# Optimization experiments

Hardware: AMD Instinct MI355X
Metric: run time of the kernel (lower is better)

Reference implementation:

```python
import jax, jax.numpy as jnp
import numpy as np

B = 4096; CPG = 2; NPC = 25              # graphs, components/graph, nodes/component
N = B * CPG * NPC; C = B * CPG; E = 409600
IN_CH = 128; HID = 256; L = 3; S = 64; M = 8; NCLS = 2
BN_EPS = 1e-5

def _leaky(x):
    return jax.nn.leaky_relu(x, 0.01)

def _gin_conv(x, src, dst, wa, ba, wb, bb):
    # GINConv with eps=0: mlp(x + sum_{j in N(i)} x_j); messages flow src->dst
    agg = jnp.zeros_like(x).at[dst].add(x[src])
    h = x + agg
    return jax.nn.relu(h @ wa + ba) @ wb + bb

def setup_inputs():
    key = jax.random.key(0)
    ks = jax.random.split(key, 12)
    rn = lambda k, shp: jax.random.normal(k, shp, jnp.float32) * 0.05
    return {
        "x": jax.random.normal(ks[0], (N, IN_CH), jnp.float32),
        "w0a": rn(ks[1], (IN_CH, HID)), "b0a": jnp.zeros((HID,), jnp.float32),
        "w0b": rn(ks[2], (HID, HID)), "b0b": jnp.zeros((HID,), jnp.float32),
        "wra": rn(ks[3], (L - 1, HID, HID)), "bra": jnp.zeros((L - 1, HID), jnp.float32),
        "wrb": rn(ks[4], (L - 1, HID, HID)), "brb": jnp.zeros((L - 1, HID), jnp.float32),
        "Wc": jax.random.uniform(ks[5], (HID, S * M), jnp.float32, -1.0, 1.0),
        "fc1_w": rn(ks[6], (S, 32)), "fc1_b": jnp.zeros((32,), jnp.float32),
        "bn_g": jnp.ones((32,), jnp.float32), "bn_b": jnp.zeros((32,), jnp.float32),
        "fc2_w": rn(ks[7], (32, NCLS)), "fc2_b": jnp.zeros((NCLS,), jnp.float32),
        "edge_index": jax.random.randint(ks[8], (2, E), 0, N, jnp.int32),
        "node2comp": (jnp.arange(N, dtype=jnp.int32) // NPC),
        "comp2graph": (jnp.arange(C, dtype=jnp.int32) // CPG),
        "comp_pos": (jnp.arange(C, dtype=jnp.int32) % CPG),
        "n_graphs": B,
        "max_comps": CPG,
    }

def reference(x, w0a, b0a, w0b, b0b, wra, bra, wrb, brb, Wc, fc1_w, fc1_b, bn_g, bn_b, fc2_w, fc2_b, edge_index, node2comp, comp2graph, comp_pos, n_graphs, max_comps):
    src, dst = edge_index[0], edge_index[1]
    # --- GIN backbone (num_layers convs, ReLU between layers) ---
    h = _gin_conv(x, src, dst, w0a, b0a, w0b, b0b)
    for i in range(wra.shape[0]):
        h = jax.nn.relu(h)
        h = _gin_conv(h, src, dst, wra[i], bra[i], wrb[i], brb[i])
    # --- per-connected-component mean pooling ---
    n_comp = comp2graph.shape[0]
    comp_sum = jax.ops.segment_sum(h, node2comp, num_segments=n_comp)           # [C, d]
    comp_size = jax.ops.segment_sum(jnp.ones((h.shape[0],), h.dtype), node2comp, num_segments=n_comp)
    # torch.mean over the zero-padded cardinality dim divides by the per-graph MAX component size
    graph_maxc = jax.ops.segment_max(comp_size, comp2graph, num_segments=n_graphs)
    comp_mean = comp_sum / graph_maxc[comp2graph][:, None]
    # --- pad components into [B, max_comps, d] ---
    X = jnp.zeros((n_graphs, max_comps, h.shape[1]), h.dtype).at[comp2graph, comp_pos].set(comp_mean)
    # --- set-rep classifier ---
    t = _leaky(jnp.einsum('bcd,dk->bck', X, Wc))                                # [B, maxC, S*M]
    s = fc1_w.shape[0]; m = Wc.shape[1] // s
    t = t.reshape(t.shape[0], t.shape[1], m, s)                                 # view(B, maxC, n_elements, n_hidden_sets)
    t = jnp.max(t, axis=2)
    t = jnp.sum(t, axis=1)                                                      # [B, S]
    t = t @ fc1_w + fc1_b
    mu = jnp.mean(t, axis=0); var = jnp.var(t, axis=0)                          # BN, batch stats (track_running_stats=False)
    t = (t - mu) / jnp.sqrt(var + BN_EPS) * bn_g + bn_b
    t = _leaky(t)
    out = t @ fc2_w + fc2_b
    return jax.nn.log_softmax(out, axis=1)
```

## Files before the change

### kernel.cpp

```cpp
#include <hip/hip_runtime.h>
#include <hip/hip_fp16.h>
#include <math.h>

typedef unsigned short u16;
typedef float f32x4 __attribute__((ext_vector_type(4)));
typedef __bf16 bf16x8 __attribute__((ext_vector_type(8)));

__device__ __forceinline__ float b2f(u16 u) {
    union { unsigned int i; float f; } v; v.i = ((unsigned int)u) << 16; return v.f;
}
__device__ __forceinline__ u16 f2b(float f) {
    union { float f; unsigned int i; } v; v.f = f;
    unsigned int lsb = (v.i >> 16) & 1u;
    return (u16)((v.i + 0x7fffu + lsb) >> 16);
}
__device__ __forceinline__ unsigned int cvtpk(float lo, float hi) {
    unsigned int r;
    asm("v_cvt_pk_bf16_f32 %0, %1, %2" : "=v"(r) : "v"(lo), "v"(hi));
    return r;
}

__global__ __launch_bounds__(256)
void k_scan1(const int* __restrict__ cnt, int* __restrict__ rowptr,
             int* __restrict__ bsum, int N)
{
    __shared__ int s[256];
    int t = threadIdx.x, i = blockIdx.x * 256 + t;
    int v = (i < N) ? cnt[i] : 0;
    s[t] = v;
    __syncthreads();
#pragma unroll
    for (int off = 1; off < 256; off <<= 1) {
        int add = (t >= off) ? s[t - off] : 0;
        __syncthreads();
        s[t] += add;
        __syncthreads();
    }
    if (i < N) rowptr[i] = s[t] - v;
    if (t == 255) bsum[blockIdx.x] = s[255];
}

__global__ __launch_bounds__(256)
void k_scan2(const int* __restrict__ bsum, int* __restrict__ bscan, int nb)
{
    __shared__ int s[256];
    int t = threadIdx.x;
    int g[4], e[4];
    int base = t * 4;
#pragma unroll
    for (int j = 0; j < 4; ++j) g[j] = (base + j < nb) ? bsum[base + j] : 0;
    e[0] = 0; e[1] = g[0]; e[2] = g[0] + g[1]; e[3] = g[0] + g[1] + g[2];
    int tsum = e[3] + g[3];
    s[t] = tsum;
    __syncthreads();
#pragma unroll
    for (int off = 1; off < 256; off <<= 1) {
        int add = (t >= off) ? s[t - off] : 0;
        __syncthreads();
        s[t] += add;
        __syncthreads();
    }
    int texcl = s[t] - tsum;
#pragma unroll
    for (int j = 0; j < 4; ++j)
        if (base + j < nb) bscan[base + j] = texcl + e[j];
}

__global__ __launch_bounds__(256)
void k_scan3(int* __restrict__ rowptr, const int* __restrict__ bscan,
             int* __restrict__ cursor, int N)
{
    int i = blockIdx.x * 256 + threadIdx.x;
    if (i >= N) return;
    int r = rowptr[i] + bscan[i >> 8];
    rowptr[i] = r;
    cursor[i] = r;
}

__global__ __launch_bounds__(256)
void k_fill(const int* __restrict__ src, const int* __restrict__ dst,
            int* __restrict__ cursor, int* __restrict__ col, int E)
{
    int e = blockIdx.x * 256 + threadIdx.x;
    if (e >= E) return;
    int pos = atomicAdd(&cursor[dst[e]], 1);
    col[pos] = src[e];
}

__global__ __launch_bounds__(256)
void k_setup(const float* __restrict__ w0a, const float* __restrict__ w0b,
             const float* __restrict__ wra, const float* __restrict__ wrb,
             const float* __restrict__ Wc,  u16* __restrict__ wt,
             const int* __restrict__ dst, int* __restrict__ cnt, int E)
{
    int t = blockIdx.x * 256 + threadIdx.x;
    if (t < E) atomicAdd(&cnt[dst[t]], 1);

    const float* in; u16* out; int K, N, l;
    if      (t < 32768)  { in = w0a;          out = wt;          K = 128; N = 256; l = t; }
    else if (t < 98304)  { in = w0b;          out = wt + 65536;  K = 256; N = 256; l = t - 32768; }
    else if (t < 163840) { in = wra;          out = wt + 131072; K = 256; N = 256; l = t - 98304; }
    else if (t < 229376) { in = wra + 65536;  out = wt + 196608; K = 256; N = 256; l = t - 163840; }
    else if (t < 294912) { in = wrb;          out = wt + 262144; K = 256; N = 256; l = t - 229376; }
    else if (t < 360448) { in = wrb + 65536;  out = wt + 327680; K = 256; N = 256; l = t - 294912; }
    else if (t < 491520) { in = Wc;           out = wt + 393216; K = 256; N = 512; l = t - 360448; }
    else return;
    out[l] = f2b(in[(l % K) * N + l / K]);
}

#define CCAP 512

template<int K, bool RELU, bool F32SRC>
__global__ __launch_bounds__(512, 6)
void k_gin(const void* __restrict__ hsrc,
           const int* __restrict__ cnt, const int* __restrict__ rowptr,
           const int* __restrict__ col,
           const u16* __restrict__ WaT, const float* __restrict__ ba,
           const u16* __restrict__ WbT, const float* __restrict__ bb,
           u16* __restrict__ Hout, int Ntot, int Etot)
{
    __shared__ u16 AH[64 * 256];
    __shared__ int colLDS[CCAP];

    const int tid = threadIdx.x, lane = tid & 63, wave = tid >> 6;
    const int bm0 = blockIdx.x * 64;
    const int lc = lane & 15, lr = (lane >> 4) * 4;
    const int cw0 = wave * 32;
    const int l15 = lane & 15, lq = lane >> 4;

    const int rp0 = rowptr[bm0];
    const int rpE = (bm0 + 64 < Ntot) ? rowptr[bm0 + 64] : Etot;
    const int total = rpE - rp0;
    for (int i = tid; i < total && i < CCAP; i += 512) colLDS[i] = col[rp0 + i];

    bf16x8 bpre0 = *(const bf16x8*)(WaT + (size_t)(cw0 + l15) * K + lq * 8);
    bf16x8 bpre1 = *(const bf16x8*)(WaT + (size_t)(cw0 + 16 + l15) * K + lq * 8);
    __syncthreads();

    {
        constexpr int NSEG = K / 8;
        const int gr = tid >> 3, gseg = tid & 7;
        const int node = bm0 + gr;
        const int nn = cnt[node], rp = rowptr[node];
        const int jbase = rp - rp0;
        const int nIt = nn + 1;

        float acc[NSEG];
#pragma unroll
        for (int i = 0; i < NSEG; ++i) acc[i] = 0.f;

        if (F32SRC) {
            const float4* bp = (const float4*)hsrc;
            const int stride = K / 4, off = gseg * (NSEG / 4);
            const float4* p = bp + (size_t)node * stride + off;
            float4 a0 = p[0], a1 = p[1];
            for (int t = 0; t < nIt; ++t) {
                float4 b0 = p[2], b1 = p[3];
                int tn = (t + 1 < nIt) ? t + 1 : t;
                int jl = jbase + tn - 1;
                int idxN = (tn == 0) ? node : ((jl < CCAP) ? colLDS[jl] : col[rp + tn - 1]);
                const float4* q = bp + (size_t)idxN * stride + off;
                float4 n0 = q[0], n1 = q[1];
                if (RELU) {
                    acc[0] += fmaxf(a0.x,0.f); acc[1] += fmaxf(a0.y,0.f); acc[2] += fmaxf(a0.z,0.f); acc[3] += fmaxf(a0.w,0.f);
                    acc[4] += fmaxf(a1.x,0.f); acc[5] += fmaxf(a1.y,0.f); acc[6] += fmaxf(a1.z,0.f); acc[7] += fmaxf(a1.w,0.f);
                    acc[8] += fmaxf(b0.x,0.f); acc[9] += fmaxf(b0.y,0.f); acc[10]+= fmaxf(b0.z,0.f); acc[11]+= fmaxf(b0.w,0.f);
                    acc[12]+= fmaxf(b1.x,0.f); acc[13]+= fmaxf(b1.y,0.f); acc[14]+= fmaxf(b1.z,0.f); acc[15]+= fmaxf(b1.w,0.f);
                } else {
                    acc[0] += a0.x; acc[1] += a0.y; acc[2] += a0.z; acc[3] += a0.w;
                    acc[4] += a1.x; acc[5] += a1.y; acc[6] += a1.z; acc[7] += a1.w;
                    acc[8] += b0.x; acc[9] += b0.y; acc[10]+= b0.z; acc[11]+= b0.w;
                    acc[12]+= b1.x; acc[13]+= b1.y; acc[14]+= b1.z; acc[15]+= b1.w;
                }
                a0 = n0; a1 = n1; p = q;
            }
        } else {
            const uint4* bp = (const uint4*)hsrc;
            const int stride = K / 8, off = gseg * (NSEG / 8);
            const uint4* p = bp + (size_t)node * stride + off;
            uint4 a0 = p[0], a1 = p[1];
            for (int t = 0; t < nIt; ++t) {
                uint4 b0 = p[2], b1 = p[3];
                int tn = (t + 1 < nIt) ? t + 1 : t;
                int jl = jbase + tn - 1;
                int idxN = (tn == 0) ? node : ((jl < CCAP) ? colLDS[jl] : col[rp + tn - 1]);
                const uint4* q = bp + (size_t)idxN * stride + off;
                uint4 n0 = q[0], n1 = q[1];
                u16 vs[32] __attribute__((aligned(16)));
                *(uint4*)(vs + 0)  = a0; *(uint4*)(vs + 8)  = a1;
                *(uint4*)(vs + 16) = b0; *(uint4*)(vs + 24) = b1;
#pragma unroll
                for (int i2 = 0; i2 < 32; ++i2) {
                    float x = b2f(vs[i2]);
                    acc[i2] += RELU ? fmaxf(x, 0.f) : x;
                }
                a0 = n0; a1 = n1; p = q;
            }
        }

        const int k0 = gseg * NSEG;
        constexpr int NKC = NSEG / 8;
#pragma unroll
        for (int cc = 0; cc < NKC; ++cc) {
            const int k = k0 + cc * 8;
            const int s  = (k >> 5) * 256 + (gr >> 4) * 64 + ((k >> 3) & 3) * 16 + (gr & 15);
            const int sp = s ^ ((k >> 5) & 7);
            uint4 pk;
            pk.x = cvtpk(acc[cc * 8 + 0], acc[cc * 8 + 1]);
            pk.y = cvtpk(acc[cc * 8 + 2], acc[cc * 8 + 3]);
            pk.z = cvtpk(acc[cc * 8 + 4], acc[cc * 8 + 5]);
            pk.w = cvtpk(acc[cc * 8 + 6], acc[cc * 8 + 7]);
            *(uint4*)(AH + sp * 8) = pk;
        }
    }
    __syncthreads();

    constexpr int NK1 = K / 32;
    f32x4 acc1[4][2];
#pragma unroll
    for (int r = 0; r < 4; ++r)
#pragma unroll
        for (int c = 0; c < 2; ++c) acc1[r][c] = (f32x4){0.f, 0.f, 0.f, 0.f};

#pragma unroll
    for (int kb = 0; kb < NK1; ++kb) {
        bf16x8 a[4], b[2];
        if (kb == 0) { b[0] = bpre0; b[1] = bpre1; }
        else {
#pragma unroll
            for (int c = 0; c < 2; ++c)
                b[c] = *(const bf16x8*)(WaT + (size_t)(cw0 + c * 16 + l15) * K + kb * 32 + lq * 8);
        }
#pragma unroll
        for (int r = 0; r < 4; ++r)
            a[r] = *(const bf16x8*)&AH[(kb * 256 + r * 64 + (lane ^ (kb & 7))) * 8];
        __builtin_amdgcn_s_setprio(1);
#pragma unroll
        for (int r = 0; r < 4; ++r)
#pragma unroll
            for (int c = 0; c < 2; ++c)
                acc1[r][c] = __builtin_amdgcn_mfma_f32_16x16x32_bf16(a[r], b[c], acc1[r][c], 0, 0, 0);
        __builtin_amdgcn_s_setprio(0);
    }
    __syncthreads();

#pragma unroll
    for (int c = 0; c < 2; ++c) {
        const int n = cw0 + c * 16 + lc;
        const float bv = ba[n];
        const int nb = (n >> 5) * 256 + ((n >> 3) & 3) * 16;
        const int sx = (n >> 5) & 7;
#pragma unroll
        for (int r = 0; r < 4; ++r)
#pragma unroll
            for (int i = 0; i < 4; ++i) {
                const int sp = (nb + r * 64 + lr + i) ^ sx;
                AH[sp * 8 + (n & 7)] = f2b(fmaxf(acc1[r][c][i] + bv, 0.f));
            }
    }
    __syncthreads();

    f32x4 acc2[4][2];
#pragma unroll
    for (int r = 0; r < 4; ++r)
#pragma unroll
        for (int c = 0; c < 2; ++c) acc2[r][c] = (f32x4){0.f, 0.f, 0.f, 0.f};

#pragma unroll
    for (int kb = 0; kb < 8; ++kb) {
        bf16x8 a[4], b[2];
#pragma unroll
        for (int c = 0; c < 2; ++c)
            b[c] = *(const bf16x8*)(WbT + (size_t)(cw0 + c * 16 + l15) * 256 + kb * 32 + lq * 8);
#pragma unroll
        for (int r = 0; r < 4; ++r)
            a[r] = *(const bf16x8*)&AH[(kb * 256 + r * 64 + (lane ^ (kb & 7))) * 8];
        __builtin_amdgcn_s_setprio(1);
#pragma unroll
        for (int r = 0; r < 4; ++r)
#pragma unroll
            for (int c = 0; c < 2; ++c)
                acc2[r][c] = __builtin_amdgcn_mfma_f32_16x16x32_bf16(a[r], b[c], acc2[r][c], 0, 0, 0);
        __builtin_amdgcn_s_setprio(0);
    }
#pragma unroll
    for (int c = 0; c < 2; ++c) {
        const int n = cw0 + c * 16 + lc;
        const float bv = bb[n];
#pragma unroll
        for (int r = 0; r < 4; ++r)
#pragma unroll
            for (int i = 0; i < 4; ++i)
                Hout[(size_t)(bm0 + r * 16 + lr + i) * 256 + n] = f2b(acc2[r][c][i] + bv);
    }
}

__global__ __launch_bounds__(256)
void k_lin(const u16* __restrict__ A, const u16* __restrict__ WT,
           float* __restrict__ C)
{
    __shared__ u16 As[64 * 40];
    __shared__ u16 Bs[256 * 40];
    const int tid = threadIdx.x, lane = tid & 63, wave = tid >> 6;
    const int bm0 = blockIdx.x * 64, bn0 = blockIdx.y * 256;
    const int fm = lane & 15, fk = (lane >> 4) * 8;
    const int lc = lane & 15, lr = (lane >> 4) * 4;
    const int cw0 = wave * 64;
    const int sr = tid >> 2, sc = tid & 3;

    f32x4 acc[4][4];
#pragma unroll
    for (int r = 0; r < 4; ++r)
#pragma unroll
        for (int c = 0; c < 4; ++c) acc[r][c] = (f32x4){0.f, 0.f, 0.f, 0.f};

    for (int k0 = 0; k0 < 256; k0 += 32) {
        *(uint4*)&As[sr * 40 + sc * 8] =
            *(const uint4*)(A + (size_t)(bm0 + sr) * 256 + k0 + sc * 8);
        {
            const uint4* wp = (const uint4*)(WT + (size_t)(bn0 + tid) * 256 + k0);
#pragma unroll
            for (int c = 0; c < 4; ++c)
                *(uint4*)&Bs[tid * 40 + c * 8] = wp[c];
        }
        __syncthreads();
        bf16x8 a[4], b[4];
#pragma unroll
        for (int r = 0; r < 4; ++r) a[r] = *(const bf16x8*)&As[(r * 16 + fm) * 40 + fk];
#pragma unroll
        for (int c = 0; c < 4; ++c) b[c] = *(const bf16x8*)&Bs[(cw0 + c * 16 + fm) * 40 + fk];
#pragma unroll
        for (int r = 0; r < 4; ++r)
#pragma unroll
            for (int c = 0; c < 4; ++c)
                acc[r][c] = __builtin_amdgcn_mfma_f32_16x16x32_bf16(a[r], b[c], acc[r][c], 0, 0, 0);
        __syncthreads();
    }
#pragma unroll
    for (int c = 0; c < 4; ++c) {
        const int col = bn0 + cw0 + c * 16 + lc;
#pragma unroll
        for (int r = 0; r < 4; ++r)
#pragma unroll
            for (int i = 0; i < 4; ++i) {
                float v = acc[r][c][i];
                v = (v >= 0.f) ? v : 0.01f * v;
                C[(size_t)(bm0 + r * 16 + lr + i) * 512 + col] = v;
            }
    }
}

__global__ void k_pool(const u16* __restrict__ H, u16* __restrict__ Xc)
{
    int c = blockIdx.x, f = threadIdx.x;
    const u16* p = H + (size_t)c * 25 * 256 + f;
    float s = 0.f;
#pragma unroll
    for (int j = 0; j < 25; ++j) s += b2f(p[j * 256]);
    Xc[(size_t)c * 256 + f] = f2b(s / 25.0f);
}

__global__ __launch_bounds__(256)
void k_sf(const float* __restrict__ T, const float* __restrict__ w,
          const float* __restrict__ b, float* __restrict__ T1)
{
    __shared__ float tp[8][64];
    const int gl = threadIdx.x >> 5, j = threadIdx.x & 31;
    const int g = blockIdx.x * 8 + gl;
#pragma unroll
    for (int h = 0; h < 2; ++h) {
        const int s = j + h * 32;
        float acc = 0.f;
#pragma unroll
        for (int c = 0; c < 2; ++c) {
            const float* row = T + ((size_t)(g * 2 + c)) * 512 + s;
            float mx = row[0];
#pragma unroll
            for (int m = 1; m < 8; ++m) mx = fmaxf(mx, row[m * 64]);
            acc += mx;
        }
        tp[gl][s] = acc;
    }
    __syncthreads();
    float sum = b[j];
#pragma unroll
    for (int k = 0; k < 64; ++k) sum += tp[gl][k] * w[k * 32 + j];
    T1[g * 32 + j] = sum;
}

__global__ void k_bnstats(const float* __restrict__ T1, float* __restrict__ stats)
{
    __shared__ float r1[256], r2[256];
    const int j = blockIdx.x, t = threadIdx.x;
    float s = 0.f, ss = 0.f;
    for (int b = t; b < 4096; b += 256) {
        float v = T1[b * 32 + j];
        s += v; ss += v * v;
    }
    r1[t] = s; r2[t] = ss;
    __syncthreads();
    for (int off = 128; off > 0; off >>= 1) {
        if (t < off) { r1[t] += r1[t + off]; r2[t] += r2[t + off]; }
        __syncthreads();
    }
    if (t == 0) {
        float mu  = r1[0] * (1.f / 4096.f);
        float var = r2[0] * (1.f / 4096.f) - mu * mu;
        stats[j]      = mu;
        stats[32 + j] = 1.f / sqrtf(var + 1e-5f);
    }
}

__global__ void k_head(const float* __restrict__ T1, const float* __restrict__ stats,
                       const float* __restrict__ g, const float* __restrict__ bb,
                       const float* __restrict__ w2, const float* __restrict__ b2,
                       float* __restrict__ out)
{
    const int b = blockIdx.x * 256 + threadIdx.x;
    float l0 = b2[0], l1 = b2[1];
#pragma unroll
    for (int j = 0; j < 32; ++j) {
        float v = (T1[b * 32 + j] - stats[j]) * stats[32 + j] * g[j] + bb[j];
        v = (v >= 0.f) ? v : 0.01f * v;
        l0 += v * w2[j * 2];
        l1 += v * w2[j * 2 + 1];
    }
    float mx  = fmaxf(l0, l1);
    float lse = mx + logf(expf(l0 - mx) + expf(l1 - mx));
    out[b * 2]     = l0 - lse;
    out[b * 2 + 1] = l1 - lse;
}

extern "C" void kernel_launch(void* const* d_in, const int* in_sizes, int n_in,
                              void* d_out, int out_size, void* d_ws, size_t ws_size,
                              hipStream_t stream)
{
    (void)n_in; (void)out_size; (void)ws_size;
    constexpr int NN = 204800, NCOMP = 8192, NGRAPH = 4096;

    const float* x    = (const float*)d_in[0];
    const float* w0a  = (const float*)d_in[1];
    const float* b0a  = (const float*)d_in[2];
    const float* w0b  = (const float*)d_in[3];
    const float* b0b  = (const float*)d_in[4];
    const float* wra  = (const float*)d_in[5];
    const float* bra  = (const float*)d_in[6];
    const float* wrb  = (const float*)d_in[7];
    const float* brb  = (const float*)d_in[8];
    const float* Wc   = (const float*)d_in[9];
    const float* f1w  = (const float*)d_in[10];
    const float* f1b  = (const float*)d_in[11];
    const float* bng  = (const float*)d_in[12];
    const float* bnb  = (const float*)d_in[13];
    const float* f2w  = (const float*)d_in[14];
    const float* f2bb = (const float*)d_in[15];
    const int* ei   = (const int*)d_in[16];
    const int  E    = in_sizes[16] / 2;
    const int* src  = ei;
    const int* dst  = ei + E;

    char* ws = (char*)d_ws;
    u16*    H1  = (u16*)ws;
    u16*    H0  = (u16*)(ws + (size_t)104857600);
    u16*    wt  = (u16*)(ws + (size_t)209715200);
    u16 *WT0 = wt, *WT1 = wt + 65536, *WT2 = wt + 131072, *WT3 = wt + 196608,
        *WT4 = wt + 262144, *WT5 = wt + 327680, *WT6 = wt + 393216;
    char* csr = ws + (size_t)210763776;
    int* cnt    = (int*)csr;
    int* rowptr = (int*)(csr + 819200);
    int* cursor = (int*)(csr + 1638400);
    int* col    = (int*)(csr + 2457600);
    int* bsum   = (int*)(csr + 4096000);
    int* bscan  = (int*)(csr + 4100096);
    u16*   Xc    = (u16*)ws;
    float* Tfull = (float*)(ws + (size_t)16777216);
    float* T1    = (float*)(ws + (size_t)41943040);
    float* stats = (float*)(ws + (size_t)46137344);

    const dim3 blk(256);
    const dim3 blk512(512);
    const int NB = NN / 256;

    hipMemsetAsync(cnt, 0, NN * 4, stream);
    k_setup<<<1920, blk, 0, stream>>>(w0a, w0b, wra, wrb, Wc, wt, dst, cnt, E);
    k_scan1<<<NB, blk, 0, stream>>>(cnt, rowptr, bsum, NN);
    k_scan2<<<1, blk, 0, stream>>>(bsum, bscan, NB);
    k_scan3<<<NB, blk, 0, stream>>>(rowptr, bscan, cursor, NN);
    k_fill<<<(E + 255) / 256, blk, 0, stream>>>(src, dst, cursor, col, E);

    k_gin<128, false, true><<<NN / 64, blk512, 0, stream>>>(
        x, cnt, rowptr, col, WT0, b0a, WT1, b0b, H0, NN, E);
    k_gin<256, true, false><<<NN / 64, blk512, 0, stream>>>(
        H0, cnt, rowptr, col, WT2, bra, WT4, brb, H1, NN, E);
    k_gin<256, true, false><<<NN / 64, blk512, 0, stream>>>(
        H1, cnt, rowptr, col, WT3, bra + 256, WT5, brb + 256, H0, NN, E);

    k_pool<<<NCOMP, blk, 0, stream>>>(H0, Xc);
    k_lin<<<dim3(NCOMP / 64, 2), blk, 0, stream>>>(Xc, WT6, Tfull);
    k_sf<<<NGRAPH / 8, blk, 0, stream>>>(Tfull, f1w, f1b, T1);
    k_bnstats<<<32, blk, 0, stream>>>(T1, stats);
    k_head<<<NGRAPH / 256, blk, 0, stream>>>(T1, stats, bng, bnb, f2w, f2bb, (float*)d_out);
}
```

Before: 687.6 us.

## Fuse component mean pooling into last GIN layer and BN stats into k_sf

The last GIN layer now stages its bf16 output tile in LDS and reduces rows per component directly, atomically adding partial sums into an fp32 component buffer. This avoids writing and re-reading the full node feature matrix, and a small finalize kernel divides by 25 and converts to bf16. BatchNorm sums and sums of squares are accumulated with atomics inside k_sf, which removes the separate stats kernel, and k_head derives mean and rstd itself. The cost is extra syncs and atomics in the GIN epilogue, two memsets, and slightly different rounding because the sums are formed in fp32 from bf16-rounded values.

```diff
diff --git a/kernel.cpp b/kernel.cpp
--- a/kernel.cpp
+++ b/kernel.cpp
@@ -110,14 +110,14 @@
 
 #define CCAP 512
 
-template<int K, bool RELU, bool F32SRC>
+template<int K, bool RELU, bool F32SRC, bool LAST>
 __global__ __launch_bounds__(512, 6)
 void k_gin(const void* __restrict__ hsrc,
            const int* __restrict__ cnt, const int* __restrict__ rowptr,
            const int* __restrict__ col,
            const u16* __restrict__ WaT, const float* __restrict__ ba,
            const u16* __restrict__ WbT, const float* __restrict__ bb,
-           u16* __restrict__ Hout, int Ntot, int Etot)
+           u16* __restrict__ Hout, float* __restrict__ Xcf, int Ntot, int Etot)
 {
     __shared__ u16 AH[64 * 256];
     __shared__ int colLDS[CCAP];
@@ -283,16 +283,52 @@
                 acc2[r][c] = __builtin_amdgcn_mfma_f32_16x16x32_bf16(a[r], b[c], acc2[r][c], 0, 0, 0);
         __builtin_amdgcn_s_setprio(0);
     }
-#pragma unroll
-    for (int c = 0; c < 2; ++c) {
-        const int n = cw0 + c * 16 + lc;
-        const float bv = bb[n];
-#pragma unroll
-        for (int r = 0; r < 4; ++r)
-#pragma unroll
-            for (int i = 0; i < 4; ++i)
-                Hout[(size_t)(bm0 + r * 16 + lr + i) * 256 + n] = f2b(acc2[r][c][i] + bv);
-    }
+
+    if (!LAST) {
+#pragma unroll
+        for (int c = 0; c < 2; ++c) {
+            const int n = cw0 + c * 16 + lc;
+            const float bv = bb[n];
+#pragma unroll
+            for (int r = 0; r < 4; ++r)
+#pragma unroll
+                for (int i = 0; i < 4; ++i)
+                    Hout[(size_t)(bm0 + r * 16 + lr + i) * 256 + n] = f2b(acc2[r][c][i] + bv);
+        }
+    } else {
+        __syncthreads();
+#pragma unroll
+        for (int c = 0; c < 2; ++c) {
+            const int n = cw0 + c * 16 + lc;
+            const float bv = bb[n];
+#pragma unroll
+            for (int r = 0; r < 4; ++r)
+#pragma unroll
+                for (int i = 0; i < 4; ++i)
+                    AH[(r * 16 + lr + i) * 256 + n] = f2b(acc2[r][c][i] + bv);
+        }
+        __syncthreads();
+        const int f = tid & 255, h = tid >> 8;
+        const int cfirst = bm0 / 25, clast = (bm0 + 63) / 25;
+        for (int cc2 = cfirst + h; cc2 <= clast; cc2 += 2) {
+            int lo = cc2 * 25 - bm0;      if (lo < 0) lo = 0;
+            int hi = cc2 * 25 + 25 - bm0; if (hi > 64) hi = 64;
+            float s2 = 0.f;
+            for (int r2 = lo; r2 < hi; ++r2) s2 += b2f(AH[r2 * 256 + f]);
+            atomicAdd(&Xcf[(size_t)cc2 * 256 + f], s2);
+        }
+    }
+}
+
+__global__ __launch_bounds__(256)
+void k_poolfin(const float* __restrict__ Xcf, u16* __restrict__ Xc)
+{
+    int t = blockIdx.x * 256 + threadIdx.x;
+    float4 v = *(const float4*)(Xcf + (size_t)t * 4);
+    u16 o[4] __attribute__((aligned(8)));
+    o[0] = f2b(v.x / 25.0f); o[1] = f2b(v.y / 25.0f);
+    o[2] = f2b(v.z / 25.0f); o[3] = f2b(v.w / 25.0f);
+    *(uint2*)(Xc + (size_t)t * 4) = *(const uint2*)o;
 }
 
 __global__ __launch_bounds__(256)
@@ -350,19 +386,10 @@
     }
 }
 
-__global__ void k_pool(const u16* __restrict__ H, u16* __restrict__ Xc)
-{
-    int c = blockIdx.x, f = threadIdx.x;
-    const u16* p = H + (size_t)c * 25 * 256 + f;
-    float s = 0.f;
-#pragma unroll
-    for (int j = 0; j < 25; ++j) s += b2f(p[j * 256]);
-    Xc[(size_t)c * 256 + f] = f2b(s / 25.0f);
-}
-
 __global__ __launch_bounds__(256)
 void k_sf(const float* __restrict__ T, const float* __restrict__ w,
-          const float* __restrict__ b, float* __restrict__ T1)
+          const float* __restrict__ b, float* __restrict__ T1,
+          float* __restrict__ stats)
 {
     __shared__ float tp[8][64];
     const int gl = threadIdx.x >> 5, j = threadIdx.x & 31;
@@ -386,28 +413,19 @@
 #pragma unroll
     for (int k = 0; k < 64; ++k) sum += tp[gl][k] * w[k * 32 + j];
     T1[g * 32 + j] = sum;
-}
-
-__global__ void k_bnstats(const float* __restrict__ T1, float* __restrict__ stats)
-{
-    __shared__ float r1[256], r2[256];
-    const int j = blockIdx.x, t = threadIdx.x;
-    float s = 0.f, ss = 0.f;
-    for (int b = t; b < 4096; b += 256) {
-        float v = T1[b * 32 + j];
-        s += v; ss += v * v;
-    }
-    r1[t] = s; r2[t] = ss;
-    __syncthreads();
-    for (int off = 128; off > 0; off >>= 1) {
-        if (t < off) { r1[t] += r1[t + off]; r2[t] += r2[t + off]; }
-        __syncthreads();
-    }
-    if (t == 0) {
-        float mu  = r1[0] * (1.f / 4096.f);
-        float var = r2[0] * (1.f / 4096.f) - mu * mu;
-        stats[j]      = mu;
-        stats[32 + j] = 1.f / sqrtf(var + 1e-5f);
+    __syncthreads();
+    float* red = &tp[0][0];
+    red[gl * 32 + j] = sum;
+    __syncthreads();
+    if (threadIdx.x < 32) {
+        float s = 0.f, ss = 0.f;
+#pragma unroll
+        for (int g2 = 0; g2 < 8; ++g2) {
+            float v = red[g2 * 32 + threadIdx.x];
+            s += v; ss += v * v;
+        }
+        atomicAdd(&stats[threadIdx.x], s);
+        atomicAdd(&stats[32 + threadIdx.x], ss);
     }
 }
 
@@ -420,7 +438,10 @@
     float l0 = b2[0], l1 = b2[1];
 #pragma unroll
     for (int j = 0; j < 32; ++j) {
-        float v = (T1[b * 32 + j] - stats[j]) * stats[32 + j] * g[j] + bb[j];
+        float mu  = stats[j] * (1.f / 4096.f);
+        float var = stats[32 + j] * (1.f / 4096.f) - mu * mu;
+        float rstd = 1.f / sqrtf(var + 1e-5f);
+        float v = (T1[b * 32 + j] - mu) * rstd * g[j] + bb[j];
         v = (v >= 0.f) ? v : 0.01f * v;
         l0 += v * w2[j * 2];
         l1 += v * w2[j * 2 + 1];
@@ -472,6 +493,7 @@
     int* col    = (int*)(csr + 2457600);
     int* bsum   = (int*)(csr + 4096000);
     int* bscan  = (int*)(csr + 4100096);
+    float* Xcf   = (float*)(ws + (size_t)104857600);
     u16*   Xc    = (u16*)ws;
     float* Tfull = (float*)(ws + (size_t)16777216);
     float* T1    = (float*)(ws + (size_t)41943040);
@@ -488,16 +510,17 @@
     k_scan3<<<NB, blk, 0, stream>>>(rowptr, bscan, cursor, NN);
     k_fill<<<(E + 255) / 256, blk, 0, stream>>>(src, dst, cursor, col, E);
 
-    k_gin<128, false, true><<<NN / 64, blk512, 0, stream>>>(
-        x, cnt, rowptr, col, WT0, b0a, WT1, b0b, H0, NN, E);
-    k_gin<256, true, false><<<NN / 64, blk512, 0, stream>>>(
-        H0, cnt, rowptr, col, WT2, bra, WT4, brb, H1, NN, E);
-    k_gin<256, true, false><<<NN / 64, blk512, 0, stream>>>(
-        H1, cnt, rowptr, col, WT3, bra + 256, WT5, brb + 256, H0, NN, E);
-
-    k_pool<<<NCOMP, blk, 0, stream>>>(H0, Xc);
+    k_gin<128, false, true, false><<<NN / 64, blk512, 0, stream>>>(
+        x, cnt, rowptr, col, WT0, b0a, WT1, b0b, H0, nullptr, NN, E);
+    k_gin<256, true, false, false><<<NN / 64, blk512, 0, stream>>>(
+        H0, cnt, rowptr, col, WT2, bra, WT4, brb, H1, nullptr, NN, E);
+    hipMemsetAsync(Xcf, 0, (size_t)NCOMP * 256 * 4, stream);
+    k_gin<256, true, false, true><<<NN / 64, blk512, 0, stream>>>(
+        H1, cnt, rowptr, col, WT3, bra + 256, WT5, brb + 256, nullptr, Xcf, NN, E);
+
+    k_poolfin<<<(NCOMP * 256 / 4) / 256, blk, 0, stream>>>(Xcf, Xc);
     k_lin<<<dim3(NCOMP / 64, 2), blk, 0, stream>>>(Xc, WT6, Tfull);
-    k_sf<<<NGRAPH / 8, blk, 0, stream>>>(Tfull, f1w, f1b, T1);
-    k_bnstats<<<32, blk, 0, stream>>>(T1, stats);
+    hipMemsetAsync(stats, 0, 256, stream);
+    k_sf<<<NGRAPH / 8, blk, 0, stream>>>(Tfull, f1w, f1b, T1, stats);
     k_head<<<NGRAPH / 256, blk, 0, stream>>>(T1, stats, bng, bnb, f2w, f2bb, (float*)d_out);
 }
```

New measurement: 684.1 us. No clear change (-0.5%).
